# Performance work log

Hardware: AMD Instinct MI355X
Metric: run time of the kernel (lower is better)

Reference implementation:

```python
import jax, jax.numpy as jnp
import numpy as np

N_NODES = 50000
N_EDGES = 400000
IN_FEATS = 1433
HID = 384
EMB = 256
N_CLS = 7


def setup_inputs() -> dict:
    key = jax.random.key(0)
    ks = jax.random.split(key, 9)
    features = jax.random.normal(ks[0], (N_NODES, IN_FEATS), jnp.float32)
    edge_src = jax.random.randint(ks[1], (N_EDGES,), 0, N_NODES)
    edge_dst = jax.random.randint(ks[2], (N_EDGES,), 0, N_NODES)
    W1 = jax.random.normal(ks[3], (IN_FEATS, HID), jnp.float32) * 0.02
    b1 = jnp.zeros((HID,), jnp.float32)
    W2 = jax.random.normal(ks[4], (HID, EMB), jnp.float32) * 0.02
    b2 = jnp.zeros((EMB,), jnp.float32)
    Wc = jax.random.normal(ks[5], (EMB, N_CLS), jnp.float32) * 0.02
    bc = jnp.zeros((N_CLS,), jnp.float32)
    return {"features": features, "edge_src": edge_src, "edge_dst": edge_dst,
            "W1": W1, "b1": b1, "W2": W2, "b2": b2, "Wc": Wc, "bc": bc}


def reference(features, edge_src, edge_dst, W1, b1, W2, b2, Wc, bc):
    N = features.shape[0]
    ones = jnp.ones(edge_src.shape[0], features.dtype)
    deg_out = jax.ops.segment_sum(ones, edge_src, num_segments=N)
    deg_in = jax.ops.segment_sum(ones, edge_dst, num_segments=N)
    inv_s = jax.lax.rsqrt(jnp.maximum(deg_out, 1.0))  # D_src^{-1/2}
    inv_d = jax.lax.rsqrt(jnp.maximum(deg_in, 1.0))   # D_dst^{-1/2}

    def gconv(x, W, b):
        # DGL GraphConv, norm='both', weight applied first (in_feats > out_feats)
        h = (x @ W) * inv_s[:, None]
        agg = jax.ops.segment_sum(h[edge_src], edge_dst, num_segments=N)
        return agg * inv_d[:, None] + b

    h = jax.nn.relu(gconv(features, W1, b1))
    h = gconv(h, W2, b2)
    return h @ Wc + bc  # [N, 7] logits
```

## Files before the change

### kernel.cpp

```cpp
#include <hip/hip_runtime.h>
#include <math.h>
#include <stdint.h>

constexpr int NNODES = 50000;
constexpr int NEDGES = 400000;
constexpr int INF = 1433;
constexpr int KP1 = 1440;
constexpr int MP1 = 50048;
constexpr int NRB = MP1 / 128;
constexpr int NKT1 = KP1 / 32;
constexpr int HID = 384;
constexpr int NKT2 = HID / 32;
constexpr int EMB = 256;
constexpr int NCLS = 7;

typedef __attribute__((ext_vector_type(8))) short bf16x8_t;
typedef __attribute__((ext_vector_type(4))) float f32x4_t;

typedef __attribute__((address_space(3))) uint32_t lds_u32_t;
typedef const __attribute__((address_space(1))) uint32_t glb_u32_t;

__global__ void degree_kernel(const int* __restrict__ src, const int* __restrict__ dst,
                              int* __restrict__ dout, int* __restrict__ din, int E) {
  int i = blockIdx.x * blockDim.x + threadIdx.x;
  int stride = gridDim.x * blockDim.x;
  for (; i < E; i += stride) {
    atomicAdd(&dout[src[i]], 1);
    atomicAdd(&din[dst[i]], 1);
  }
}

__global__ void inv_kernel(const int* __restrict__ dout, const int* __restrict__ din,
                           float* __restrict__ inv_s, float* __restrict__ inv_d, int N) {
  int i = blockIdx.x * blockDim.x + threadIdx.x;
  if (i < N) {
    inv_s[i] = 1.0f / sqrtf(fmaxf((float)dout[i], 1.0f));
    inv_d[i] = 1.0f / sqrtf(fmaxf((float)din[i], 1.0f));
  }
}

__global__ __launch_bounds__(1024)
void scan_kernel(const int* __restrict__ deg, int* __restrict__ off, int N) {
  __shared__ int buf[1024];
  __shared__ int carry;
  if (threadIdx.x == 0) carry = 0;
  __syncthreads();
  for (int base = 0; base < N; base += 1024) {
    int i = base + threadIdx.x;
    int v = (i < N) ? deg[i] : 0;
    buf[threadIdx.x] = v;
    __syncthreads();
    #pragma unroll
    for (int d = 1; d < 1024; d <<= 1) {
      int t = (threadIdx.x >= d) ? buf[threadIdx.x - d] : 0;
      __syncthreads();
      buf[threadIdx.x] += t;
      __syncthreads();
    }
    if (i < N) off[i] = carry + buf[threadIdx.x] - v;
    __syncthreads();
    if (threadIdx.x == 1023) carry += buf[1023];
    __syncthreads();
  }
  if (threadIdx.x == 0) off[N] = carry;
}

__global__ void fill_csr(const int* __restrict__ src, const int* __restrict__ dst,
                         const int* __restrict__ off, int* __restrict__ cursor,
                         int* __restrict__ csr_src, int E) {
  int i = blockIdx.x * blockDim.x + threadIdx.x;
  int stride = gridDim.x * blockDim.x;
  for (; i < E; i += stride) {
    int d = dst[i];
    int p = atomicAdd(&cursor[d], 1);
    csr_src[off[d] + p] = src[i];
  }
}

__device__ __forceinline__ uint32_t split_pack(float v) {
  uint32_t u = __float_as_uint(v);
  float hiF = __uint_as_float(u & 0xFFFF0000u);
  uint32_t u2 = __float_as_uint(v - hiF);
  return (u2 & 0xFFFF0000u) | (u >> 16);
}

__global__ void convA(const float* __restrict__ A, uint32_t* __restrict__ Ap) {
  int k4 = blockIdx.x * 256 + threadIdx.x;
  int r = blockIdx.y;
  if (k4 >= KP1 / 4) return;
  int k = k4 * 4;
  uint4 o = {0, 0, 0, 0};
  if (r < NNODES) {
    const float* row = A + (size_t)r * INF;
    if (k + 3 < INF) {
      float a0 = row[k], a1 = row[k + 1], a2 = row[k + 2], a3 = row[k + 3];
      o.x = split_pack(a0); o.y = split_pack(a1); o.z = split_pack(a2); o.w = split_pack(a3);
    } else {
      if (k + 0 < INF) o.x = split_pack(row[k + 0]);
      if (k + 1 < INF) o.y = split_pack(row[k + 1]);
      if (k + 2 < INF) o.z = split_pack(row[k + 2]);
      if (k + 3 < INF) o.w = split_pack(row[k + 3]);
    }
  }
  *(uint4*)&Ap[(size_t)r * KP1 + k] = o;
}

template<int KDIM, int NDIM, int NKTILES>
__global__ void convB(const float* __restrict__ W, char* __restrict__ Bp) {
  int T = blockIdx.x, cb = blockIdx.y;
  int kk = threadIdx.x & 31, c0 = threadIdx.x >> 5;
  char* tile = Bp + ((size_t)cb * NKTILES + T) * 16384;
  int gk = T * 32 + kk;
  #pragma unroll
  for (int i = 0; i < 16; ++i) {
    int c = c0 + i * 8;
    float v = (gk < KDIM) ? W[(size_t)gk * NDIM + cb * 128 + c] : 0.f;
    uint32_t p = split_pack(v);
    int bo = (c * 64 + kk * 2) ^ ((c & 7) << 4);
    *(ushort*)(tile + bo)        = (ushort)(p & 0xFFFFu);
    *(ushort*)(tile + 8192 + bo) = (ushort)(p >> 16);
  }
}

template<int KPD, int NOUT, int NCOLB, int NKTILES>
__global__ __launch_bounds__(256, 2)
void gemm_mfma(const uint32_t* __restrict__ Ap, const char* __restrict__ Bp,
               float* __restrict__ C, const float* __restrict__ scale)
{
  __shared__ __align__(16) char sA[16384];
  __shared__ __align__(16) char sB[16384];

  constexpr int NWG = NCOLB * NRB;
  constexpr int q = NWG / 8, rr = NWG % 8;
  int orig = blockIdx.x;
  int xcd = orig & 7, sub = orig >> 3;
  int logical = (xcd < rr ? xcd * (q + 1) : rr * (q + 1) + (xcd - rr) * q) + sub;
  int bx = logical % NCOLB;
  int by = logical / NCOLB;
  const int row0 = by * 128, col0 = bx * 128;

  const int tid = threadIdx.x;
  const int w = tid >> 6, l = tid & 63;
  const int wr = w >> 1, wc = w & 1;
  const int lane15 = l & 15, kg = l >> 4;

  size_t a_src[4];
  #pragma unroll
  for (int i = 0; i < 4; ++i) {
    int p = w * 4096 + i * 1024 + l * 16;
    int r = p >> 7;
    int kb = (p & 127) ^ ((r & 7) << 4);
    a_src[i] = ((size_t)(row0 + r) * KPD) * 4 + kb;
  }
  const char* Ab = (const char*)Ap;
  const char* Btile = Bp + (size_t)(bx * NKTILES) * 16384;

  f32x4_t acc[4][4];
  #pragma unroll
  for (int mi = 0; mi < 4; ++mi)
    #pragma unroll
    for (int ni = 0; ni < 4; ++ni) acc[mi][ni] = {0.f, 0.f, 0.f, 0.f};

  for (int T = 0; T < NKTILES; ++T) {
    #pragma unroll
    for (int i = 0; i < 4; ++i) {
      __builtin_amdgcn_global_load_lds(
          (glb_u32_t*)(Ab + a_src[i] + (size_t)T * 128),
          (lds_u32_t*)(sA + w * 4096 + i * 1024), 16, 0, 0);
    }
    #pragma unroll
    for (int i = 0; i < 4; ++i) {
      int p = w * 4096 + i * 1024;
      __builtin_amdgcn_global_load_lds(
          (glb_u32_t*)(Btile + (size_t)T * 16384 + p + l * 16),
          (lds_u32_t*)(sB + p), 16, 0, 0);
    }
    __syncthreads();

    bf16x8_t bh[4], bl[4];
    #pragma unroll
    for (int ni = 0; ni < 4; ++ni) {
      int c = wc * 64 + ni * 16 + lane15;
      int bo = (c * 64 + kg * 16) ^ ((c & 7) << 4);
      bh[ni] = *(const bf16x8_t*)(sB + bo);
      bl[ni] = *(const bf16x8_t*)(sB + 8192 + bo);
    }
    #pragma unroll
    for (int mi = 0; mi < 4; ++mi) {
      int ra = wr * 64 + mi * 16 + lane15;
      int a0 = (ra * 128 + kg * 32) ^ ((ra & 7) << 4);
      uint4 d0 = *(const uint4*)(sA + a0);
      uint4 d1 = *(const uint4*)(sA + (a0 ^ 16));
      union { uint32_t u[4]; bf16x8_t v; } th, tl;
      th.u[0] = (d0.x & 0xFFFFu) | (d0.y << 16);
      th.u[1] = (d0.z & 0xFFFFu) | (d0.w << 16);
      th.u[2] = (d1.x & 0xFFFFu) | (d1.y << 16);
      th.u[3] = (d1.z & 0xFFFFu) | (d1.w << 16);
      tl.u[0] = (d0.x >> 16) | (d0.y & 0xFFFF0000u);
      tl.u[1] = (d0.z >> 16) | (d0.w & 0xFFFF0000u);
      tl.u[2] = (d1.x >> 16) | (d1.y & 0xFFFF0000u);
      tl.u[3] = (d1.z >> 16) | (d1.w & 0xFFFF0000u);
      #pragma unroll
      for (int ni = 0; ni < 4; ++ni) {
        acc[mi][ni] = __builtin_amdgcn_mfma_f32_16x16x32_bf16(th.v, bh[ni], acc[mi][ni], 0, 0, 0);
        acc[mi][ni] = __builtin_amdgcn_mfma_f32_16x16x32_bf16(th.v, bl[ni], acc[mi][ni], 0, 0, 0);
        acc[mi][ni] = __builtin_amdgcn_mfma_f32_16x16x32_bf16(tl.v, bh[ni], acc[mi][ni], 0, 0, 0);
      }
    }
    __syncthreads();
  }

  #pragma unroll
  for (int mi = 0; mi < 4; ++mi) {
    #pragma unroll
    for (int j = 0; j < 4; ++j) {
      int gr = row0 + wr * 64 + mi * 16 + kg * 4 + j;
      if (gr >= NNODES) continue;
      float s = scale[gr];
      #pragma unroll
      for (int ni = 0; ni < 4; ++ni) {
        int gc = col0 + wc * 64 + ni * 16 + lane15;
        C[(size_t)gr * NOUT + gc] = acc[mi][ni][j] * s;
      }
    }
  }
}

template<int BK>
__global__ __launch_bounds__(256)
void gemm_scale(const float* __restrict__ A, const float* __restrict__ B,
                float* __restrict__ C, const float* __restrict__ scale,
                int M, int N, int K)
{
  constexpr int BM = 128, BN = 128;
  constexpr int LDA = BM + 4;
  constexpr int LDB = BN + 4;
  __shared__ float As[BK][LDA];
  __shared__ float Bs[BK][LDB];

  const int tid = threadIdx.x;
  const int tx = tid & 15;
  const int ty = tid >> 4;
  const int row0 = blockIdx.y * BM;
  const int col0 = blockIdx.x * BN;

  float acc[8][8];
  #pragma unroll
  for (int i = 0; i < 8; ++i)
    #pragma unroll
    for (int j = 0; j < 8; ++j) acc[i][j] = 0.f;

  for (int kt = 0; kt < K; kt += BK) {
    #pragma unroll
    for (int p = 0; p < BM / 16; ++p) {
      int r = (tid >> 4) + p * 16;
      int k = tid & 15;
      int gr = row0 + r, gk = kt + k;
      float v = 0.f;
      if (gr < M && gk < K) v = A[(size_t)gr * K + gk];
      As[k][r] = v;
    }
    #pragma unroll
    for (int p = 0; p < BK / 8; ++p) {
      int r = (tid >> 5) + p * 8;
      int c4 = (tid & 31) * 4;
      int gk = kt + r;
      float4 v = {0.f, 0.f, 0.f, 0.f};
      if (gk < K) v = *(const float4*)&B[(size_t)gk * N + col0 + c4];
      *(float4*)&Bs[r][c4] = v;
    }
    __syncthreads();
    #pragma unroll
    for (int k = 0; k < BK; ++k) {
      float4 a0 = *(const float4*)&As[k][ty * 8];
      float4 a1 = *(const float4*)&As[k][ty * 8 + 4];
      float4 b0 = *(const float4*)&Bs[k][tx * 8];
      float4 b1 = *(const float4*)&Bs[k][tx * 8 + 4];
      float av[8] = {a0.x, a0.y, a0.z, a0.w, a1.x, a1.y, a1.z, a1.w};
      float bv[8] = {b0.x, b0.y, b0.z, b0.w, b1.x, b1.y, b1.z, b1.w};
      #pragma unroll
      for (int i = 0; i < 8; ++i)
        #pragma unroll
        for (int j = 0; j < 8; ++j)
          acc[i][j] = fmaf(av[i], bv[j], acc[i][j]);
    }
    __syncthreads();
  }
  #pragma unroll
  for (int i = 0; i < 8; ++i) {
    int gr = row0 + ty * 8 + i;
    if (gr >= M) continue;
    float s = scale[gr];
    #pragma unroll
    for (int j = 0; j < 8; j += 4) {
      float4 v = {acc[i][j] * s, acc[i][j + 1] * s, acc[i][j + 2] * s, acc[i][j + 3] * s};
      *(float4*)&C[(size_t)gr * N + col0 + tx * 8 + j] = v;
    }
  }
}

template<int NF, bool RELU>
__global__ __launch_bounds__(256)
void gather_nodes(const int* __restrict__ off, const int* __restrict__ csr_src,
                  const float* __restrict__ h, const float* __restrict__ inv_d,
                  const float* __restrict__ bias, float* __restrict__ outbuf, int N)
{
  int node = blockIdx.x * 4 + (threadIdx.x >> 6);
  int lane = threadIdx.x & 63;
  if (node >= N) return;
  constexpr int NI = NF / 128;
  float2 acc[NI];
  #pragma unroll
  for (int i = 0; i < NI; ++i) acc[i] = {0.f, 0.f};

  int e0 = off[node], e1 = off[node + 1];
  for (int e = e0; e < e1; ++e) {
    const float* hr = h + (size_t)csr_src[e] * NF;
    #pragma unroll
    for (int i = 0; i < NI; ++i) {
      float2 v = *(const float2*)&hr[lane * 2 + i * 128];
      acc[i].x += v.x; acc[i].y += v.y;
    }
  }
  float s = inv_d[node];
  float* orow = outbuf + (size_t)node * NF;
  #pragma unroll
  for (int i = 0; i < NI; ++i) {
    int f = lane * 2 + i * 128;
    float2 v;
    v.x = fmaf(acc[i].x, s, bias[f]);
    v.y = fmaf(acc[i].y, s, bias[f + 1]);
    if (RELU) { v.x = fmaxf(v.x, 0.f); v.y = fmaxf(v.y, 0.f); }
    *(float2*)&orow[f] = v;
  }
}

__global__ __launch_bounds__(256)
void gather_pack(const int* __restrict__ off, const int* __restrict__ csr_src,
                 const float* __restrict__ h, const float* __restrict__ inv_d,
                 const float* __restrict__ bias, uint32_t* __restrict__ outp, int N)
{
  int node = blockIdx.x * 4 + (threadIdx.x >> 6);
  int lane = threadIdx.x & 63;
  if (node >= N) return;
  float2 acc[3];
  #pragma unroll
  for (int i = 0; i < 3; ++i) acc[i] = {0.f, 0.f};

  int e0 = off[node], e1 = off[node + 1];
  for (int e = e0; e < e1; ++e) {
    const float* hr = h + (size_t)csr_src[e] * HID;
    #pragma unroll
    for (int i = 0; i < 3; ++i) {
      float2 v = *(const float2*)&hr[lane * 2 + i * 128];
      acc[i].x += v.x; acc[i].y += v.y;
    }
  }
  float s = inv_d[node];
  uint32_t* orow = outp + (size_t)node * HID;
  #pragma unroll
  for (int i = 0; i < 3; ++i) {
    int f = lane * 2 + i * 128;
    float vx = fmaxf(fmaf(acc[i].x, s, bias[f]), 0.f);
    float vy = fmaxf(fmaf(acc[i].y, s, bias[f + 1]), 0.f);
    uint2 o = {split_pack(vx), split_pack(vy)};
    *(uint2*)&orow[f] = o;
  }
}

__global__ __launch_bounds__(256)
void gather_classifier(const int* __restrict__ off, const int* __restrict__ csr_src,
                       const float* __restrict__ h, const float* __restrict__ inv_d,
                       const float* __restrict__ b2, const float* __restrict__ Wc,
                       const float* __restrict__ bc, float* __restrict__ out, int N)
{
  __shared__ float sWc[EMB * NCLS];
  for (int i = threadIdx.x; i < EMB * NCLS; i += 256) sWc[i] = Wc[i];
  __syncthreads();

  int node = blockIdx.x * 4 + (threadIdx.x >> 6);
  int lane = threadIdx.x & 63;
  if (node >= N) return;

  float2 acc[2] = {{0.f, 0.f}, {0.f, 0.f}};
  int e0 = off[node], e1 = off[node + 1];
  for (int e = e0; e < e1; ++e) {
    const float* hr = h + (size_t)csr_src[e] * EMB;
    #pragma unroll
    for (int i = 0; i < 2; ++i) {
      float2 v = *(const float2*)&hr[lane * 2 + i * 128];
      acc[i].x += v.x; acc[i].y += v.y;
    }
  }
  float s = inv_d[node];
  float c[NCLS];
  #pragma unroll
  for (int k = 0; k < NCLS; ++k) c[k] = 0.f;
  #pragma unroll
  for (int i = 0; i < 2; ++i) {
    int f = lane * 2 + i * 128;
    float hx = fmaf(acc[i].x, s, b2[f]);
    float hy = fmaf(acc[i].y, s, b2[f + 1]);
    #pragma unroll
    for (int k = 0; k < NCLS; ++k)
      c[k] += hx * sWc[f * NCLS + k] + hy * sWc[(f + 1) * NCLS + k];
  }
  #pragma unroll
  for (int k = 0; k < NCLS; ++k) {
    float v = c[k];
    #pragma unroll
    for (int o = 32; o > 0; o >>= 1) v += __shfl_down(v, o);
    if (lane == 0) out[(size_t)node * NCLS + k] = v + bc[k];
  }
}

extern "C" void kernel_launch(void* const* d_in, const int* in_sizes, int n_in,
                              void* d_out, int out_size, void* d_ws, size_t ws_size,
                              hipStream_t stream) {
  const float* features = (const float*)d_in[0];
  const int*   esrc     = (const int*)d_in[1];
  const int*   edst     = (const int*)d_in[2];
  const float* W1       = (const float*)d_in[3];
  const float* b1       = (const float*)d_in[4];
  const float* W2       = (const float*)d_in[5];
  const float* b2       = (const float*)d_in[6];
  const float* Wc       = (const float*)d_in[7];
  const float* bc       = (const float*)d_in[8];
  float* out = (float*)d_out;

  int* deg_out = (int*)d_ws;
  int* deg_in  = deg_out + NNODES;
  int* cursor  = deg_in + NNODES;
  int* row_off = cursor + NNODES;
  int* csr_src = row_off + NNODES + 1;
  float* inv_s = (float*)(csr_src + NEDGES);
  float* inv_d = inv_s + NNODES;
  uintptr_t p16 = ((uintptr_t)(inv_d + NNODES) + 15) & ~(uintptr_t)15;
  uint32_t* hp = (uint32_t*)p16;
  float* bufA = (float*)(hp + (size_t)MP1 * HID);
  char*  Bp1  = (char*)(bufA + (size_t)NNODES * HID);
  char*  Bp2  = Bp1 + (size_t)3 * NKT1 * 16384;
  uint32_t* Ap = (uint32_t*)(Bp2 + (size_t)2 * NKT2 * 16384);

  size_t required = (uintptr_t)(Ap + (size_t)MP1 * KP1) - (uintptr_t)d_ws;
  bool use_mfma = ws_size >= required;

  hipMemsetAsync(deg_out, 0, 3 * NNODES * sizeof(int), stream);
  degree_kernel<<<1024, 256, 0, stream>>>(esrc, edst, deg_out, deg_in, NEDGES);
  inv_kernel<<<(NNODES + 255) / 256, 256, 0, stream>>>(deg_out, deg_in, inv_s, inv_d, NNODES);
  scan_kernel<<<1, 1024, 0, stream>>>(deg_in, row_off, NNODES);
  fill_csr<<<1024, 256, 0, stream>>>(esrc, edst, row_off, cursor, csr_src, NEDGES);

  if (use_mfma) {
    convA<<<dim3((KP1 / 4 + 255) / 256, MP1), 256, 0, stream>>>(features, Ap);
    convB<INF, HID, NKT1><<<dim3(NKT1, 3), 256, 0, stream>>>(W1, Bp1);
    gemm_mfma<KP1, HID, 3, NKT1><<<3 * NRB, 256, 0, stream>>>(Ap, Bp1, bufA, inv_s);
    gather_pack<<<(NNODES + 3) / 4, 256, 0, stream>>>(
        row_off, csr_src, bufA, inv_d, b1, hp, NNODES);

    convB<HID, EMB, NKT2><<<dim3(NKT2, 2), 256, 0, stream>>>(W2, Bp2);
    gemm_mfma<HID, EMB, 2, NKT2><<<2 * NRB, 256, 0, stream>>>(hp, Bp2, bufA, inv_s);
  } else {
    gemm_scale<16><<<dim3(HID / 128, (NNODES + 127) / 128), 256, 0, stream>>>(
        features, W1, bufA, inv_s, NNODES, HID, INF);
    gather_nodes<HID, true><<<(NNODES + 3) / 4, 256, 0, stream>>>(
        row_off, csr_src, bufA, inv_d, b1, (float*)hp, NNODES);
    gemm_scale<16><<<dim3(EMB / 128, (NNODES + 127) / 128), 256, 0, stream>>>(
        (float*)hp, W2, bufA, inv_s, NNODES, EMB, HID);
  }

  gather_classifier<<<(NNODES + 3) / 4, 256, 0, stream>>>(
      row_off, csr_src, bufA, inv_d, b2, Wc, bc, out, NNODES);
}
```

Baseline: 1.036 ms.

## Parallelize CSR offset scan, unroll edge gathers by four, use 32-bit GEMM offsets

Replaces the single-block serial prefix scan over 50000 degrees with a three-kernel multi-block scan (per-block scan, scan of block totals, add-back). It unrolls the edge loops in both gather kernels by four so that several neighbor rows are loaded at once. It also switches the GEMM A-tile address arithmetic from 64-bit to 32-bit offsets to cut address computation. The cost is two extra kernel launches, and the 32-bit offsets depend on the buffer staying under 4 GB.

```diff
diff --git a/kernel.cpp b/kernel.cpp
--- a/kernel.cpp
+++ b/kernel.cpp
@@ -13,6 +13,7 @@
 constexpr int NKT2 = HID / 32;
 constexpr int EMB = 256;
 constexpr int NCLS = 7;
+constexpr int NSB = (NNODES + 255) / 256;
 
 typedef __attribute__((ext_vector_type(8))) short bf16x8_t;
 typedef __attribute__((ext_vector_type(4))) float f32x4_t;
@@ -39,30 +40,47 @@
   }
 }
 
-__global__ __launch_bounds__(1024)
-void scan_kernel(const int* __restrict__ deg, int* __restrict__ off, int N) {
-  __shared__ int buf[1024];
-  __shared__ int carry;
-  if (threadIdx.x == 0) carry = 0;
+__global__ __launch_bounds__(256)
+void scan_block(const int* __restrict__ deg, int* __restrict__ off,
+                int* __restrict__ bsum, int N) {
+  __shared__ int buf[256];
+  int i = blockIdx.x * 256 + threadIdx.x;
+  int v = (i < N) ? deg[i] : 0;
+  buf[threadIdx.x] = v;
   __syncthreads();
-  for (int base = 0; base < N; base += 1024) {
-    int i = base + threadIdx.x;
-    int v = (i < N) ? deg[i] : 0;
-    buf[threadIdx.x] = v;
-    __syncthreads();
-    #pragma unroll
-    for (int d = 1; d < 1024; d <<= 1) {
-      int t = (threadIdx.x >= d) ? buf[threadIdx.x - d] : 0;
-      __syncthreads();
-      buf[threadIdx.x] += t;
-      __syncthreads();
-    }
-    if (i < N) off[i] = carry + buf[threadIdx.x] - v;
-    __syncthreads();
-    if (threadIdx.x == 1023) carry += buf[1023];
-    __syncthreads();
-  }
-  if (threadIdx.x == 0) off[N] = carry;
+  #pragma unroll
+  for (int d = 1; d < 256; d <<= 1) {
+    int t = (threadIdx.x >= d) ? buf[threadIdx.x - d] : 0;
+    __syncthreads();
+    buf[threadIdx.x] += t;
+    __syncthreads();
+  }
+  if (i < N) off[i] = buf[threadIdx.x] - v;
+  if (threadIdx.x == 255) bsum[blockIdx.x] = buf[255];
+}
+
+__global__ __launch_bounds__(256)
+void scan_tops(const int* __restrict__ bsum, int* __restrict__ boff,
+               int* __restrict__ off, int nb, int N) {
+  __shared__ int buf[256];
+  int v = (threadIdx.x < nb) ? bsum[threadIdx.x] : 0;
+  buf[threadIdx.x] = v;
+  __syncthreads();
+  #pragma unroll
+  for (int d = 1; d < 256; d <<= 1) {
+    int t = (threadIdx.x >= d) ? buf[threadIdx.x - d] : 0;
+    __syncthreads();
+    buf[threadIdx.x] += t;
+    __syncthreads();
+  }
+  if (threadIdx.x < nb) boff[threadIdx.x] = buf[threadIdx.x] - v;
+  if (threadIdx.x == 255) off[N] = buf[255];
+}
+
+__global__ __launch_bounds__(256)
+void scan_add(const int* __restrict__ boff, int* __restrict__ off, int N) {
+  int i = blockIdx.x * 256 + threadIdx.x;
+  if (i < N) off[i] += boff[blockIdx.x];
 }
 
 __global__ void fill_csr(const int* __restrict__ src, const int* __restrict__ dst,
@@ -144,13 +162,13 @@
   const int wr = w >> 1, wc = w & 1;
   const int lane15 = l & 15, kg = l >> 4;
 
-  size_t a_src[4];
+  uint32_t a_off[4];
   #pragma unroll
   for (int i = 0; i < 4; ++i) {
     int p = w * 4096 + i * 1024 + l * 16;
     int r = p >> 7;
     int kb = (p & 127) ^ ((r & 7) << 4);
-    a_src[i] = ((size_t)(row0 + r) * KPD) * 4 + kb;
+    a_off[i] = (uint32_t)(row0 + r) * (KPD * 4) + kb;
   }
   const char* Ab = (const char*)Ap;
   const char* Btile = Bp + (size_t)(bx * NKTILES) * 16384;
@@ -165,7 +183,7 @@
     #pragma unroll
     for (int i = 0; i < 4; ++i) {
       __builtin_amdgcn_global_load_lds(
-          (glb_u32_t*)(Ab + a_src[i] + (size_t)T * 128),
+          (glb_u32_t*)(Ab + (size_t)(a_off[i] + (uint32_t)T * 128u)),
           (lds_u32_t*)(sA + w * 4096 + i * 1024), 16, 0, 0);
     }
     #pragma unroll
@@ -348,7 +366,24 @@
   for (int i = 0; i < 3; ++i) acc[i] = {0.f, 0.f};
 
   int e0 = off[node], e1 = off[node + 1];
-  for (int e = e0; e < e1; ++e) {
+  int e = e0;
+  for (; e + 4 <= e1; e += 4) {
+    const float* r0 = h + (size_t)csr_src[e + 0] * HID;
+    const float* r1 = h + (size_t)csr_src[e + 1] * HID;
+    const float* r2 = h + (size_t)csr_src[e + 2] * HID;
+    const float* r3 = h + (size_t)csr_src[e + 3] * HID;
+    #pragma unroll
+    for (int i = 0; i < 3; ++i) {
+      int f = lane * 2 + i * 128;
+      float2 v0 = *(const float2*)&r0[f];
+      float2 v1 = *(const float2*)&r1[f];
+      float2 v2 = *(const float2*)&r2[f];
+      float2 v3 = *(const float2*)&r3[f];
+      acc[i].x += (v0.x + v1.x) + (v2.x + v3.x);
+      acc[i].y += (v0.y + v1.y) + (v2.y + v3.y);
+    }
+  }
+  for (; e < e1; ++e) {
     const float* hr = h + (size_t)csr_src[e] * HID;
     #pragma unroll
     for (int i = 0; i < 3; ++i) {
@@ -384,7 +419,24 @@
 
   float2 acc[2] = {{0.f, 0.f}, {0.f, 0.f}};
   int e0 = off[node], e1 = off[node + 1];
-  for (int e = e0; e < e1; ++e) {
+  int e = e0;
+  for (; e + 4 <= e1; e += 4) {
+    const float* r0 = h + (size_t)csr_src[e + 0] * EMB;
+    const float* r1 = h + (size_t)csr_src[e + 1] * EMB;
+    const float* r2 = h + (size_t)csr_src[e + 2] * EMB;
+    const float* r3 = h + (size_t)csr_src[e + 3] * EMB;
+    #pragma unroll
+    for (int i = 0; i < 2; ++i) {
+      int f = lane * 2 + i * 128;
+      float2 v0 = *(const float2*)&r0[f];
+      float2 v1 = *(const float2*)&r1[f];
+      float2 v2 = *(const float2*)&r2[f];
+      float2 v3 = *(const float2*)&r3[f];
+      acc[i].x += (v0.x + v1.x) + (v2.x + v3.x);
+      acc[i].y += (v0.y + v1.y) + (v2.y + v3.y);
+    }
+  }
+  for (; e < e1; ++e) {
     const float* hr = h + (size_t)csr_src[e] * EMB;
     #pragma unroll
     for (int i = 0; i < 2; ++i) {
@@ -433,7 +485,9 @@
   int* cursor  = deg_in + NNODES;
   int* row_off = cursor + NNODES;
   int* csr_src = row_off + NNODES + 1;
-  float* inv_s = (float*)(csr_src + NEDGES);
+  int* bsum    = csr_src + NEDGES;
+  int* boff    = bsum + NSB;
+  float* inv_s = (float*)(boff + NSB);
   float* inv_d = inv_s + NNODES;
   uintptr_t p16 = ((uintptr_t)(inv_d + NNODES) + 15) & ~(uintptr_t)15;
   uint32_t* hp = (uint32_t*)p16;
@@ -448,7 +502,9 @@
   hipMemsetAsync(deg_out, 0, 3 * NNODES * sizeof(int), stream);
   degree_kernel<<<1024, 256, 0, stream>>>(esrc, edst, deg_out, deg_in, NEDGES);
   inv_kernel<<<(NNODES + 255) / 256, 256, 0, stream>>>(deg_out, deg_in, inv_s, inv_d, NNODES);
-  scan_kernel<<<1, 1024, 0, stream>>>(deg_in, row_off, NNODES);
+  scan_block<<<NSB, 256, 0, stream>>>(deg_in, row_off, bsum, NNODES);
+  scan_tops<<<1, 256, 0, stream>>>(bsum, boff, row_off, NSB, NNODES);
+  scan_add<<<NSB, 256, 0, stream>>>(boff, row_off, NNODES);
   fill_csr<<<1024, 256, 0, stream>>>(esrc, edst, row_off, cursor, csr_src, NEDGES);
 
   if (use_mfma) {
```

After: 940.4 us. -9.2%, faster.
